# Performance work log

Hardware: AMD Instinct MI355X
Metric: run time of the kernel (lower is better)

The kernel has to match this reference:

```python
import jax, jax.numpy as jnp
import numpy as np

B, T, H, C = 131072, 40, 40, 4  # batch, seq_len (=input_size), hidden_size, classes


def setup_inputs() -> dict:
    key = jax.random.key(0)
    ks = jax.random.split(key, 7)
    s = 1.0 / np.sqrt(H)  # PyTorch LSTM/Linear init scale
    x = jax.random.normal(ks[0], (B, T), dtype=jnp.float32)
    W_ih = jax.random.uniform(ks[1], (4 * H, 1), jnp.float32, -s, s)
    W_hh = jax.random.uniform(ks[2], (4 * H, H), jnp.float32, -s, s)
    b_ih = jax.random.uniform(ks[3], (4 * H,), jnp.float32, -s, s)
    b_hh = jax.random.uniform(ks[4], (4 * H,), jnp.float32, -s, s)
    W_fc = jax.random.uniform(ks[5], (C, H), jnp.float32, -s, s)
    b_fc = jax.random.uniform(ks[6], (C,), jnp.float32, -s, s)
    return {"x": x, "W_ih": W_ih, "W_hh": W_hh, "b_ih": b_ih, "b_hh": b_hh,
            "W_fc": W_fc, "b_fc": b_fc}


def _lstm_last_hidden(x, W_ih, W_hh, b_ih, b_hh):
    # x: [B, T] -> per-step input is scalar feature. PyTorch gate order: i, f, g, o.
    b = b_ih + b_hh  # [4H]
    w_in = W_ih[:, 0]  # [4H] since input_size == 1
    h0 = jnp.zeros((x.shape[0], H), dtype=x.dtype)
    c0 = jnp.zeros((x.shape[0], H), dtype=x.dtype)

    def step(carry, x_t):
        h, c = carry
        # gates: [B, 4H]
        g = x_t[:, None] * w_in[None, :] + h @ W_hh.T + b
        i, f, gg, o = jnp.split(g, 4, axis=1)
        i = jax.nn.sigmoid(i)
        f = jax.nn.sigmoid(f)
        gg = jnp.tanh(gg)
        o = jax.nn.sigmoid(o)
        c_new = f * c + i * gg
        h_new = o * jnp.tanh(c_new)
        return (h_new, c_new), None

    (h_T, _), _ = jax.lax.scan(step, (h0, c0), x.T)  # scan over time (T steps)
    return h_T  # [B, H]


def reference(x, W_ih, W_hh, b_ih, b_hh, W_fc, b_fc):
    # Dropout(0.2) is identity in eval mode.
    h_T = _lstm_last_hidden(x, W_ih, W_hh, b_ih, b_hh)
    logits = h_T @ W_fc.T + b_fc  # [B, C]
    return logits, jnp.argmax(logits, axis=1)
```

## Files before the change

kernel.cpp:

```cpp
#include <hip/hip_runtime.h>


#define B_    131072
#define T_    40
#define H_    40
#define C_    4
#define BLK   256
#define WPB   4
#define SPW   16
#define SPB   64
#define LROW  68
#define NT    12
#define LOG2E 1.44269504088896340736f

typedef __fp16   fp16x2 __attribute__((ext_vector_type(2)));
typedef _Float16 half2v __attribute__((ext_vector_type(2)));
typedef _Float16 half4v __attribute__((ext_vector_type(4)));
typedef _Float16 half8v __attribute__((ext_vector_type(8)));
typedef float    f32x2  __attribute__((ext_vector_type(2)));
typedef float    f32x4  __attribute__((ext_vector_type(4)));

__device__ __forceinline__ float fexp2f(float v){ return __builtin_amdgcn_exp2f(v); }
__device__ __forceinline__ float frcpf (float v){ return __builtin_amdgcn_rcpf(v); }

__device__ __forceinline__ f32x2 fexp2v(f32x2 v){ return (f32x2){fexp2f(v[0]), fexp2f(v[1])}; }
__device__ __forceinline__ f32x2 frcpv (f32x2 v){ return (f32x2){frcpf(v[0]),  frcpf(v[1])};  }

__device__ __forceinline__ half2v pkrtz(float a, float b) {
    fp16x2 r = __builtin_amdgcn_cvt_pkrtz(a, b);
    return __builtin_bit_cast(half2v, r);
}

__device__ __forceinline__ float himask(float v) {
    return __builtin_bit_cast(float, __builtin_bit_cast(unsigned int, v) & 0xFFFFE000u);
}

__global__ __launch_bounds__(BLK, 2)
void lstm_mfma_kernel(const float* __restrict__ x,
                      const float* __restrict__ W_ih,
                      const float* __restrict__ W_hh,
                      const float* __restrict__ b_ih,
                      const float* __restrict__ b_hh,
                      const float* __restrict__ W_fc,
                      const float* __restrict__ b_fc,
                      float* __restrict__ out)
{
    __shared__ float lds[WPB * SPW * LROW];

    const int tid  = threadIdx.x;
    const int wv   = __builtin_amdgcn_readfirstlane(tid >> 6);
    const int lane = tid & 63;
    const int col  = lane & 15;
    const int quad = lane >> 4;
    const int sbase = blockIdx.x * SPB + wv * SPW;

    float* hbase = lds + wv * (SPW * LROW);

#pragma unroll
    for (int i = 0; i < (SPW * LROW) / 64; ++i)
        hbase[i * 64 + lane] = 0.0f;
    if (quad == 0) hbase[col * LROW + 41] = 1.0f;

    half8v Bh32[NT], Bl32[NT];
    half4v Bh16[NT], Bl16[NT];
#pragma unroll
    for (int tau = 0; tau < NT; ++tau) {
        const int   tt    = tau / 3;
        const int   ubase = (tau % 3) * 16;
        const float scale = (tt == 2) ? (2.0f * LOG2E) : (-LOG2E);
        const int   u     = ubase + col;
        const bool  valid = (u < H_);
        const int   r     = tt * H_ + (valid ? u : (H_ - 1));

        {
            float4 w0 = *reinterpret_cast<const float4*>(W_hh + r * H_ + 8 * quad);
            float4 w1 = *reinterpret_cast<const float4*>(W_hh + r * H_ + 8 * quad + 4);
            float wa[8] = {w0.x, w0.y, w0.z, w0.w, w1.x, w1.y, w1.z, w1.w};
            half8v bh, bl;
#pragma unroll
            for (int j = 0; j < 8; ++j) {
                float w = valid ? (wa[j] * scale) : 0.0f;
                _Float16 hi = (_Float16)w;
                bh[j] = hi;
                bl[j] = (_Float16)(w - (float)hi);
            }
            Bh32[tau] = bh; Bl32[tau] = bl;
        }
        {
            float4 wv4;
            if (quad == 0)      wv4 = *reinterpret_cast<const float4*>(W_hh + r * H_ + 32);
            else if (quad == 1) wv4 = *reinterpret_cast<const float4*>(W_hh + r * H_ + 36);
            else if (quad == 2) wv4 = make_float4(W_ih[r], b_ih[r] + b_hh[r], 0.0f, 0.0f);
            else                wv4 = make_float4(0.0f, 0.0f, 0.0f, 0.0f);
            float wa[4] = {wv4.x, wv4.y, wv4.z, wv4.w};
            half4v bh, bl;
#pragma unroll
            for (int j = 0; j < 4; ++j) {
                float w = valid ? (wa[j] * scale) : 0.0f;
                _Float16 hi = (_Float16)w;
                bh[j] = hi;
                bl[j] = (_Float16)(w - (float)hi);
            }
            Bh16[tau] = bh; Bl16[tau] = bl;
        }
    }

    f32x2 cst2[3][2];
#pragma unroll
    for (int jt = 0; jt < 3; ++jt) {
        cst2[jt][0] = (f32x2){0.f, 0.f};
        cst2[jt][1] = (f32x2){0.f, 0.f};
    }

    const f32x4 zc = (f32x4){0.f, 0.f, 0.f, 0.f};

    const float* myrow = hbase + col * LROW;
    const float* a32p  = myrow + 8 * quad;
    const float* a16p  = myrow + 32 + 4 * quad;
    float* xslot  = hbase + col * LROW + 40;
    float* wbase  = hbase + 4 * quad * LROW + col;
    float* wbase2 = wbase + ((col >= 8) ? 8 : 0);

    const float* xrow = x + (long)(sbase + col) * T_;
    float xv = xrow[0];

#pragma unroll 1
    for (int t = 0; t < T_; ++t) {
        if (quad == 0) *xslot = xv;
        const int tn = (t + 1 < T_) ? (t + 1) : (T_ - 1);
        const float xnext = xrow[tn];

        half8v ah32, al32; half4v ah16, al16;
        {
            f32x4 hv0 = *reinterpret_cast<const f32x4*>(a32p);
            f32x4 hv1 = *reinterpret_cast<const f32x4*>(a32p + 4);
            f32x4 hv2 = *reinterpret_cast<const f32x4*>(a16p);

            f32x4 hi0, hi1, hi2;
#pragma unroll
            for (int j = 0; j < 4; ++j) {
                hi0[j] = himask(hv0[j]);
                hi1[j] = himask(hv1[j]);
                hi2[j] = himask(hv2[j]);
            }
            f32x4 lo0 = hv0 - hi0;
            f32x4 lo1 = hv1 - hi1;
            f32x4 lo2 = hv2 - hi2;

            half2v h00 = pkrtz(hi0[0], hi0[1]);
            half2v h01 = pkrtz(hi0[2], hi0[3]);
            half2v h10 = pkrtz(hi1[0], hi1[1]);
            half2v h11 = pkrtz(hi1[2], hi1[3]);
            half2v l00 = pkrtz(lo0[0], lo0[1]);
            half2v l01 = pkrtz(lo0[2], lo0[3]);
            half2v l10 = pkrtz(lo1[0], lo1[1]);
            half2v l11 = pkrtz(lo1[2], lo1[3]);
            half2v h20 = pkrtz(hi2[0], hi2[1]);
            half2v h21 = pkrtz(hi2[2], hi2[3]);
            half2v l20 = pkrtz(lo2[0], lo2[1]);
            half2v l21 = pkrtz(lo2[2], lo2[3]);

            half4v a0 = __builtin_shufflevector(h00, h01, 0, 1, 2, 3);
            half4v a1 = __builtin_shufflevector(h10, h11, 0, 1, 2, 3);
            ah32 = __builtin_shufflevector(a0, a1, 0, 1, 2, 3, 4, 5, 6, 7);
            half4v b0 = __builtin_shufflevector(l00, l01, 0, 1, 2, 3);
            half4v b1 = __builtin_shufflevector(l10, l11, 0, 1, 2, 3);
            al32 = __builtin_shufflevector(b0, b1, 0, 1, 2, 3, 4, 5, 6, 7);
            ah16 = __builtin_shufflevector(h20, h21, 0, 1, 2, 3);
            al16 = __builtin_shufflevector(l20, l21, 0, 1, 2, 3);
        }

#pragma unroll
        for (int jt = 0; jt < 3; ++jt) {
#define DOT48(tau, dst)                                                          \
            {                                                                    \
                f32x4 a = __builtin_amdgcn_mfma_f32_16x16x32_f16(ah32, Bh32[tau], zc, 0, 0, 0); \
                a = __builtin_amdgcn_mfma_f32_16x16x32_f16(al32, Bh32[tau], a, 0, 0, 0); \
                a = __builtin_amdgcn_mfma_f32_16x16x32_f16(ah32, Bl32[tau], a, 0, 0, 0); \
                a = __builtin_amdgcn_mfma_f32_16x16x16f16(ah16, Bh16[tau], a, 0, 0, 0); \
                a = __builtin_amdgcn_mfma_f32_16x16x16f16(al16, Bh16[tau], a, 0, 0, 0); \
                a = __builtin_amdgcn_mfma_f32_16x16x16f16(ah16, Bl16[tau], a, 0, 0, 0); \
                dst = a;                                                         \
            }
            f32x4 ai, af, ag, ao;
            DOT48(jt, ai)
            DOT48(3 + jt, af)
            DOT48(6 + jt, ag)
            DOT48(9 + jt, ao)
#undef DOT48

#pragma unroll
            for (int p = 0; p < 2; ++p) {
                const f32x2 yi = (f32x2){ai[2*p], ai[2*p+1]};
                const f32x2 yf = (f32x2){af[2*p], af[2*p+1]};
                const f32x2 yg = (f32x2){ag[2*p], ag[2*p+1]};
                const f32x2 yo = (f32x2){ao[2*p], ao[2*p+1]};
                const f32x2 ei = fexp2v(yi);
                const f32x2 ef = fexp2v(yf);
                const f32x2 Eg = fexp2v(yg);
                const f32x2 eo = fexp2v(yo);
                const f32x2 one = (f32x2){1.0f, 1.0f};
                const f32x2 u_ = one + ei;
                const f32x2 v_ = one + Eg;
                const f32x2 w_ = one + ef;
                const f32x2 p_ = u_ * v_;
                const f32x2 q_ = (Eg - one) * w_;
                const f32x2 num = cst2[jt][p] * p_ + q_;
                const f32x2 cn  = num * frcpv(p_ * w_);
                cst2[jt][p] = cn;
                const f32x2 Ec = fexp2v(cn * (f32x2){2.0f*LOG2E, 2.0f*LOG2E});
                const f32x2 hn = (Ec - one) * frcpv((one + eo) * (one + Ec));
                if (jt < 2) {
                    wbase [(2*p)   * LROW + jt * 16] = hn[0];
                    wbase [(2*p+1) * LROW + jt * 16] = hn[1];
                } else {
                    wbase2[(2*p)   * LROW + 32]      = hn[0];
                    wbase2[(2*p+1) * LROW + 32]      = hn[1];
                }
            }
        }

        xv = xnext;
    }

    {
        float acc = b_fc[quad];
#pragma unroll
        for (int jj = 0; jj < 10; ++jj) {
            f32x4 hv = *reinterpret_cast<const f32x4*>(myrow + 4 * jj);
            float4 wv4 = *reinterpret_cast<const float4*>(W_fc + quad * H_ + 4 * jj);
            acc = fmaf(hv[0], wv4.x, acc);
            acc = fmaf(hv[1], wv4.y, acc);
            acc = fmaf(hv[2], wv4.z, acc);
            acc = fmaf(hv[3], wv4.w, acc);
        }
        out[(long)(sbase + col) * C_ + quad] = acc;
        hbase[col * LROW + 56 + quad] = acc;
    }
    if (quad == 0) {
        f32x4 lg = *reinterpret_cast<const f32x4*>(hbase + col * LROW + 56);
        int am = 0;
        float best = lg[0];
        if (lg[1] > best) { best = lg[1]; am = 1; }
        if (lg[2] > best) { best = lg[2]; am = 2; }
        if (lg[3] > best) { best = lg[3]; am = 3; }
        out[(long)B_ * C_ + sbase + col] = (float)am;
    }
}

extern "C" void kernel_launch(void* const* d_in, const int* in_sizes, int n_in,
                              void* d_out, int out_size, void* d_ws, size_t ws_size,
                              hipStream_t stream) {
    const float* x    = (const float*)d_in[0];
    const float* W_ih = (const float*)d_in[1];
    const float* W_hh = (const float*)d_in[2];
    const float* b_ih = (const float*)d_in[3];
    const float* b_hh = (const float*)d_in[4];
    const float* W_fc = (const float*)d_in[5];
    const float* b_fc = (const float*)d_in[6];
    float* out = (float*)d_out;

    dim3 block(BLK);
    dim3 grid(B_ / SPB);
    hipLaunchKernelGGL(lstm_mfma_kernel, grid, block, 0, stream,
                       x, W_ih, W_hh, b_ih, b_hh, W_fc, b_fc, out);
}
```

Measured before the change: 411.0 us.

## Process four independent 16-sample tiles per wave to interleave MFMA chains

Each wave now handles four independent 16-sample chunks at once, and loops twice over groups of them. The MFMA and activation work of the separate chains can interleave, hiding the dependency latency of each step's MFMA chain. The recurrent weight fragments are reused across more samples per load. The costs are higher register and LDS pressure, occupancy dropping to one block per SIMD budget, and fewer blocks in the grid.

New measurement: 456.4 us. +11.0%, slower.

```diff
diff --git a/kernel.cpp b/kernel.cpp
--- a/kernel.cpp
+++ b/kernel.cpp
@@ -7,9 +7,12 @@
 #define C_    4
 #define BLK   256
 #define WPB   4
-#define SPW   16
-#define SPB   64
-#define LROW  68
+#define NCH   4
+#define NGRP  2
+#define SPW   (NCH * 16)
+#define SPB   (WPB * SPW * NGRP)
+#define LROW  60
+#define TILEF (16 * LROW)
 #define NT    12
 #define LOG2E 1.44269504088896340736f
 
@@ -35,7 +38,85 @@
     return __builtin_bit_cast(float, __builtin_bit_cast(unsigned int, v) & 0xFFFFE000u);
 }
 
-__global__ __launch_bounds__(BLK, 2)
+__device__ __forceinline__ void prep_frags(const float* p32, const float* p16,
+                                           half8v& ah32, half8v& al32,
+                                           half4v& ah16, half4v& al16)
+{
+    f32x4 hv0 = *reinterpret_cast<const f32x4*>(p32);
+    f32x4 hv1 = *reinterpret_cast<const f32x4*>(p32 + 4);
+    f32x4 hv2 = *reinterpret_cast<const f32x4*>(p16);
+
+    f32x4 hi0, hi1, hi2;
+#pragma unroll
+    for (int j = 0; j < 4; ++j) {
+        hi0[j] = himask(hv0[j]);
+        hi1[j] = himask(hv1[j]);
+        hi2[j] = himask(hv2[j]);
+    }
+    f32x4 lo0 = hv0 - hi0;
+    f32x4 lo1 = hv1 - hi1;
+    f32x4 lo2 = hv2 - hi2;
+
+    half2v h00 = pkrtz(hi0[0], hi0[1]);
+    half2v h01 = pkrtz(hi0[2], hi0[3]);
+    half2v h10 = pkrtz(hi1[0], hi1[1]);
+    half2v h11 = pkrtz(hi1[2], hi1[3]);
+    half2v l00 = pkrtz(lo0[0], lo0[1]);
+    half2v l01 = pkrtz(lo0[2], lo0[3]);
+    half2v l10 = pkrtz(lo1[0], lo1[1]);
+    half2v l11 = pkrtz(lo1[2], lo1[3]);
+    half2v h20 = pkrtz(hi2[0], hi2[1]);
+    half2v h21 = pkrtz(hi2[2], hi2[3]);
+    half2v l20 = pkrtz(lo2[0], lo2[1]);
+    half2v l21 = pkrtz(lo2[2], lo2[3]);
+
+    half4v a0 = __builtin_shufflevector(h00, h01, 0, 1, 2, 3);
+    half4v a1 = __builtin_shufflevector(h10, h11, 0, 1, 2, 3);
+    ah32 = __builtin_shufflevector(a0, a1, 0, 1, 2, 3, 4, 5, 6, 7);
+    half4v b0 = __builtin_shufflevector(l00, l01, 0, 1, 2, 3);
+    half4v b1 = __builtin_shufflevector(l10, l11, 0, 1, 2, 3);
+    al32 = __builtin_shufflevector(b0, b1, 0, 1, 2, 3, 4, 5, 6, 7);
+    ah16 = __builtin_shufflevector(h20, h21, 0, 1, 2, 3);
+    al16 = __builtin_shufflevector(l20, l21, 0, 1, 2, 3);
+}
+
+__device__ __forceinline__ void gates_act(const f32x4& ai, const f32x4& af,
+                                          const f32x4& ag, const f32x4& ao,
+                                          f32x2 (&cst)[2],
+                                          float* wb, float* wb2, const int jt)
+{
+#pragma unroll
+    for (int p = 0; p < 2; ++p) {
+        const f32x2 yi = (f32x2){ai[2*p], ai[2*p+1]};
+        const f32x2 yf = (f32x2){af[2*p], af[2*p+1]};
+        const f32x2 yg = (f32x2){ag[2*p], ag[2*p+1]};
+        const f32x2 yo = (f32x2){ao[2*p], ao[2*p+1]};
+        const f32x2 ei = fexp2v(yi);
+        const f32x2 ef = fexp2v(yf);
+        const f32x2 Eg = fexp2v(yg);
+        const f32x2 eo = fexp2v(yo);
+        const f32x2 one = (f32x2){1.0f, 1.0f};
+        const f32x2 u_ = one + ei;
+        const f32x2 v_ = one + Eg;
+        const f32x2 w_ = one + ef;
+        const f32x2 p_ = u_ * v_;
+        const f32x2 q_ = (Eg - one) * w_;
+        const f32x2 num = cst[p] * p_ + q_;
+        const f32x2 cn  = num * frcpv(p_ * w_);
+        cst[p] = cn;
+        const f32x2 Ec = fexp2v(cn * (f32x2){2.0f*LOG2E, 2.0f*LOG2E});
+        const f32x2 hn = (Ec - one) * frcpv((one + eo) * (one + Ec));
+        if (jt < 2) {
+            wb [(2*p)   * LROW + jt * 16] = hn[0];
+            wb [(2*p+1) * LROW + jt * 16] = hn[1];
+        } else {
+            wb2[(2*p)   * LROW + 32]      = hn[0];
+            wb2[(2*p+1) * LROW + 32]      = hn[1];
+        }
+    }
+}
+
+__global__ __launch_bounds__(BLK, 1)
 void lstm_mfma_kernel(const float* __restrict__ x,
                       const float* __restrict__ W_ih,
                       const float* __restrict__ W_hh,
@@ -45,21 +126,15 @@
                       const float* __restrict__ b_fc,
                       float* __restrict__ out)
 {
-    __shared__ float lds[WPB * SPW * LROW];
+    __shared__ __align__(16) float lds[WPB * NCH * TILEF];
 
     const int tid  = threadIdx.x;
     const int wv   = __builtin_amdgcn_readfirstlane(tid >> 6);
     const int lane = tid & 63;
     const int col  = lane & 15;
     const int quad = lane >> 4;
-    const int sbase = blockIdx.x * SPB + wv * SPW;
-
-    float* hbase = lds + wv * (SPW * LROW);
-
-#pragma unroll
-    for (int i = 0; i < (SPW * LROW) / 64; ++i)
-        hbase[i * 64 + lane] = 0.0f;
-    if (quad == 0) hbase[col * LROW + 41] = 1.0f;
+
+    float* hbase = lds + wv * (NCH * TILEF);
 
     half8v Bh32[NT], Bl32[NT];
     half4v Bh16[NT], Bl16[NT];
@@ -105,146 +180,108 @@
         }
     }
 
-    f32x2 cst2[3][2];
-#pragma unroll
-    for (int jt = 0; jt < 3; ++jt) {
-        cst2[jt][0] = (f32x2){0.f, 0.f};
-        cst2[jt][1] = (f32x2){0.f, 0.f};
-    }
-
     const f32x4 zc = (f32x4){0.f, 0.f, 0.f, 0.f};
 
-    const float* myrow = hbase + col * LROW;
-    const float* a32p  = myrow + 8 * quad;
-    const float* a16p  = myrow + 32 + 4 * quad;
-    float* xslot  = hbase + col * LROW + 40;
-    float* wbase  = hbase + 4 * quad * LROW + col;
-    float* wbase2 = wbase + ((col >= 8) ? 8 : 0);
-
-    const float* xrow = x + (long)(sbase + col) * T_;
-    float xv = xrow[0];
+    const float* pA   = hbase + col * LROW + 8 * quad;
+    const float* pA16 = hbase + col * LROW + 32 + 4 * quad;
+    float* pX   = hbase + quad * TILEF + col * LROW + 40;
+    float* pW   = hbase + 4 * quad * LROW + col;
+    float* pW2  = pW + ((col >= 8) ? 8 : 0);
+    float* pRow = hbase + col * LROW;
+
+    const long wavebase = (long)blockIdx.x * SPB + (long)wv * (SPW * NGRP);
 
 #pragma unroll 1
-    for (int t = 0; t < T_; ++t) {
-        if (quad == 0) *xslot = xv;
-        const int tn = (t + 1 < T_) ? (t + 1) : (T_ - 1);
-        const float xnext = xrow[tn];
-
-        half8v ah32, al32; half4v ah16, al16;
+    for (int g = 0; g < NGRP; ++g) {
+        const long gbase = wavebase + (long)g * SPW;
+
         {
-            f32x4 hv0 = *reinterpret_cast<const f32x4*>(a32p);
-            f32x4 hv1 = *reinterpret_cast<const f32x4*>(a32p + 4);
-            f32x4 hv2 = *reinterpret_cast<const f32x4*>(a16p);
-
-            f32x4 hi0, hi1, hi2;
-#pragma unroll
-            for (int j = 0; j < 4; ++j) {
-                hi0[j] = himask(hv0[j]);
-                hi1[j] = himask(hv1[j]);
-                hi2[j] = himask(hv2[j]);
-            }
-            f32x4 lo0 = hv0 - hi0;
-            f32x4 lo1 = hv1 - hi1;
-            f32x4 lo2 = hv2 - hi2;
-
-            half2v h00 = pkrtz(hi0[0], hi0[1]);
-            half2v h01 = pkrtz(hi0[2], hi0[3]);
-            half2v h10 = pkrtz(hi1[0], hi1[1]);
-            half2v h11 = pkrtz(hi1[2], hi1[3]);
-            half2v l00 = pkrtz(lo0[0], lo0[1]);
-            half2v l01 = pkrtz(lo0[2], lo0[3]);
-            half2v l10 = pkrtz(lo1[0], lo1[1]);
-            half2v l11 = pkrtz(lo1[2], lo1[3]);
-            half2v h20 = pkrtz(hi2[0], hi2[1]);
-            half2v h21 = pkrtz(hi2[2], hi2[3]);
-            half2v l20 = pkrtz(lo2[0], lo2[1]);
-            half2v l21 = pkrtz(lo2[2], lo2[3]);
-
-            half4v a0 = __builtin_shufflevector(h00, h01, 0, 1, 2, 3);
-            half4v a1 = __builtin_shufflevector(h10, h11, 0, 1, 2, 3);
-            ah32 = __builtin_shufflevector(a0, a1, 0, 1, 2, 3, 4, 5, 6, 7);
-            half4v b0 = __builtin_shufflevector(l00, l01, 0, 1, 2, 3);
-            half4v b1 = __builtin_shufflevector(l10, l11, 0, 1, 2, 3);
-            al32 = __builtin_shufflevector(b0, b1, 0, 1, 2, 3, 4, 5, 6, 7);
-            ah16 = __builtin_shufflevector(h20, h21, 0, 1, 2, 3);
-            al16 = __builtin_shufflevector(l20, l21, 0, 1, 2, 3);
-        }
-
-#pragma unroll
-        for (int jt = 0; jt < 3; ++jt) {
+            f32x4* zp = reinterpret_cast<f32x4*>(hbase);
+#pragma unroll
+            for (int i = 0; i < (NCH * TILEF) / 4 / 64; ++i)
+                zp[i * 64 + lane] = zc;
+            hbase[quad * TILEF + col * LROW + 41] = 1.0f;
+        }
+
+        f32x2 cst2[NCH][3][2];
+#pragma unroll
+        for (int c = 0; c < NCH; ++c)
+#pragma unroll
+            for (int jt = 0; jt < 3; ++jt) {
+                cst2[c][jt][0] = (f32x2){0.f, 0.f};
+                cst2[c][jt][1] = (f32x2){0.f, 0.f};
+            }
+
+        const float* xs = x + (long)(gbase + quad * 16 + col) * T_;
+        float xv = xs[0];
+
+#pragma unroll 1
+        for (int t = 0; t < T_; ++t) {
+            *pX = xv;
+            const int tn = (t + 1 < T_) ? (t + 1) : (T_ - 1);
+            const float xnext = xs[tn];
+
+            half8v ah32[NCH], al32[NCH]; half4v ah16[NCH], al16[NCH];
+#pragma unroll
+            for (int c = 0; c < NCH; ++c)
+                prep_frags(pA + c * TILEF, pA16 + c * TILEF,
+                           ah32[c], al32[c], ah16[c], al16[c]);
+
+#pragma unroll
+            for (int jt = 0; jt < 3; ++jt) {
+#pragma unroll
+                for (int c = 0; c < NCH; ++c) {
 #define DOT48(tau, dst)                                                          \
-            {                                                                    \
-                f32x4 a = __builtin_amdgcn_mfma_f32_16x16x32_f16(ah32, Bh32[tau], zc, 0, 0, 0); \
-                a = __builtin_amdgcn_mfma_f32_16x16x32_f16(al32, Bh32[tau], a, 0, 0, 0); \
-                a = __builtin_amdgcn_mfma_f32_16x16x32_f16(ah32, Bl32[tau], a, 0, 0, 0); \
-                a = __builtin_amdgcn_mfma_f32_16x16x16f16(ah16, Bh16[tau], a, 0, 0, 0); \
-                a = __builtin_amdgcn_mfma_f32_16x16x16f16(al16, Bh16[tau], a, 0, 0, 0); \
-                a = __builtin_amdgcn_mfma_f32_16x16x16f16(ah16, Bl16[tau], a, 0, 0, 0); \
-                dst = a;                                                         \
-            }
-            f32x4 ai, af, ag, ao;
-            DOT48(jt, ai)
-            DOT48(3 + jt, af)
-            DOT48(6 + jt, ag)
-            DOT48(9 + jt, ao)
+                    {                                                            \
+                        f32x4 a_ = __builtin_amdgcn_mfma_f32_16x16x32_f16(ah32[c], Bh32[tau], zc, 0, 0, 0); \
+                        a_ = __builtin_amdgcn_mfma_f32_16x16x32_f16(al32[c], Bh32[tau], a_, 0, 0, 0); \
+                        a_ = __builtin_amdgcn_mfma_f32_16x16x32_f16(ah32[c], Bl32[tau], a_, 0, 0, 0); \
+                        a_ = __builtin_amdgcn_mfma_f32_16x16x16f16(ah16[c], Bh16[tau], a_, 0, 0, 0); \
+                        a_ = __builtin_amdgcn_mfma_f32_16x16x16f16(al16[c], Bh16[tau], a_, 0, 0, 0); \
+                        a_ = __builtin_amdgcn_mfma_f32_16x16x16f16(ah16[c], Bl16[tau], a_, 0, 0, 0); \
+                        dst = a_;                                                \
+                    }
+                    f32x4 ai, af, ag, ao;
+                    DOT48(jt,     ai)
+                    DOT48(3 + jt, af)
+                    DOT48(6 + jt, ag)
+                    DOT48(9 + jt, ao)
 #undef DOT48
-
-#pragma unroll
-            for (int p = 0; p < 2; ++p) {
-                const f32x2 yi = (f32x2){ai[2*p], ai[2*p+1]};
-                const f32x2 yf = (f32x2){af[2*p], af[2*p+1]};
-                const f32x2 yg = (f32x2){ag[2*p], ag[2*p+1]};
-                const f32x2 yo = (f32x2){ao[2*p], ao[2*p+1]};
-                const f32x2 ei = fexp2v(yi);
-                const f32x2 ef = fexp2v(yf);
-                const f32x2 Eg = fexp2v(yg);
-                const f32x2 eo = fexp2v(yo);
-                const f32x2 one = (f32x2){1.0f, 1.0f};
-                const f32x2 u_ = one + ei;
-                const f32x2 v_ = one + Eg;
-                const f32x2 w_ = one + ef;
-                const f32x2 p_ = u_ * v_;
-                const f32x2 q_ = (Eg - one) * w_;
-                const f32x2 num = cst2[jt][p] * p_ + q_;
-                const f32x2 cn  = num * frcpv(p_ * w_);
-                cst2[jt][p] = cn;
-                const f32x2 Ec = fexp2v(cn * (f32x2){2.0f*LOG2E, 2.0f*LOG2E});
-                const f32x2 hn = (Ec - one) * frcpv((one + eo) * (one + Ec));
-                if (jt < 2) {
-                    wbase [(2*p)   * LROW + jt * 16] = hn[0];
-                    wbase [(2*p+1) * LROW + jt * 16] = hn[1];
-                } else {
-                    wbase2[(2*p)   * LROW + 32]      = hn[0];
-                    wbase2[(2*p+1) * LROW + 32]      = hn[1];
+                    gates_act(ai, af, ag, ao, cst2[c][jt],
+                              pW + c * TILEF, pW2 + c * TILEF, jt);
                 }
             }
-        }
-
-        xv = xnext;
-    }
-
-    {
-        float acc = b_fc[quad];
-#pragma unroll
-        for (int jj = 0; jj < 10; ++jj) {
-            f32x4 hv = *reinterpret_cast<const f32x4*>(myrow + 4 * jj);
-            float4 wv4 = *reinterpret_cast<const float4*>(W_fc + quad * H_ + 4 * jj);
-            acc = fmaf(hv[0], wv4.x, acc);
-            acc = fmaf(hv[1], wv4.y, acc);
-            acc = fmaf(hv[2], wv4.z, acc);
-            acc = fmaf(hv[3], wv4.w, acc);
-        }
-        out[(long)(sbase + col) * C_ + quad] = acc;
-        hbase[col * LROW + 56 + quad] = acc;
-    }
-    if (quad == 0) {
-        f32x4 lg = *reinterpret_cast<const f32x4*>(hbase + col * LROW + 56);
-        int am = 0;
-        float best = lg[0];
-        if (lg[1] > best) { best = lg[1]; am = 1; }
-        if (lg[2] > best) { best = lg[2]; am = 2; }
-        if (lg[3] > best) { best = lg[3]; am = 3; }
-        out[(long)B_ * C_ + sbase + col] = (float)am;
+
+            xv = xnext;
+        }
+
+#pragma unroll
+        for (int c = 0; c < NCH; ++c) {
+            float acc = b_fc[quad];
+#pragma unroll
+            for (int jj = 0; jj < 10; ++jj) {
+                f32x4 hv = *reinterpret_cast<const f32x4*>(pRow + c * TILEF + 4 * jj);
+                float4 wv4 = *reinterpret_cast<const float4*>(W_fc + quad * H_ + 4 * jj);
+                acc = fmaf(hv[0], wv4.x, acc);
+                acc = fmaf(hv[1], wv4.y, acc);
+                acc = fmaf(hv[2], wv4.z, acc);
+                acc = fmaf(hv[3], wv4.w, acc);
+            }
+            out[(long)(gbase + c * 16 + col) * C_ + quad] = acc;
+            pRow[c * TILEF + 56 + quad] = acc;
+        }
+        if (quad == 0) {
+#pragma unroll
+            for (int c = 0; c < NCH; ++c) {
+                f32x4 lg = *reinterpret_cast<const f32x4*>(pRow + c * TILEF + 56);
+                int am = 0;
+                float best = lg[0];
+                if (lg[1] > best) { best = lg[1]; am = 1; }
+                if (lg[2] > best) { best = lg[2]; am = 2; }
+                if (lg[3] > best) { best = lg[3]; am = 3; }
+                out[(long)B_ * C_ + gbase + c * 16 + col] = (float)am;
+            }
+        }
     }
 }
 
```

## Pack tail hidden units into two gate tiles and reload h early

Applied to the files above, without the earlier changes.

The last 8 hidden units (32..39) are now packed so that one 16-column MFMA tile carries the i and f gates and another carries g and o, with lane-xor-8 shuffles exchanging the partner values. This cuts the weight tiles from 12 to 10, which removes two 6-MFMA groups per timestep that previously ran on padded zero columns. The next step's h loads are also moved up to right after the LDS writes they depend on, and the x slot store is moved, so the loads can overlap with the remaining math. The cost is cross-lane shuffles and more subtle ordering. Reading LDS without barriers relies on the per-wave layout, and the earlier loads must stay ordered after the matching writes.

Result: faster. 381.1 us (-7.3%).

```diff
diff --git a/kernel.cpp b/kernel.cpp
--- a/kernel.cpp
+++ b/kernel.cpp
@@ -10,7 +10,7 @@
 #define SPW   16
 #define SPB   64
 #define LROW  68
-#define NT    12
+#define NT    10
 #define LOG2E 1.44269504088896340736f
 
 typedef __fp16   fp16x2 __attribute__((ext_vector_type(2)));
@@ -26,6 +26,10 @@
 __device__ __forceinline__ f32x2 fexp2v(f32x2 v){ return (f32x2){fexp2f(v[0]), fexp2f(v[1])}; }
 __device__ __forceinline__ f32x2 frcpv (f32x2 v){ return (f32x2){frcpf(v[0]),  frcpf(v[1])};  }
 
+__device__ __forceinline__ f32x2 shflx8(f32x2 v){
+    return (f32x2){ __shfl_xor(v[0], 8, 64), __shfl_xor(v[1], 8, 64) };
+}
+
 __device__ __forceinline__ half2v pkrtz(float a, float b) {
     fp16x2 r = __builtin_amdgcn_cvt_pkrtz(a, b);
     return __builtin_bit_cast(half2v, r);
@@ -33,6 +37,37 @@
 
 __device__ __forceinline__ float himask(float v) {
     return __builtin_bit_cast(float, __builtin_bit_cast(unsigned int, v) & 0xFFFFE000u);
+}
+
+__device__ __forceinline__ void gates_act(const f32x4& ai, const f32x4& af,
+                                          const f32x4& ag, const f32x4& ao,
+                                          f32x2 (&cst)[2],
+                                          float* wb, const int jt)
+{
+#pragma unroll
+    for (int p = 0; p < 2; ++p) {
+        const f32x2 yi = (f32x2){ai[2*p], ai[2*p+1]};
+        const f32x2 yf = (f32x2){af[2*p], af[2*p+1]};
+        const f32x2 yg = (f32x2){ag[2*p], ag[2*p+1]};
+        const f32x2 yo = (f32x2){ao[2*p], ao[2*p+1]};
+        const f32x2 ei = fexp2v(yi);
+        const f32x2 ef = fexp2v(yf);
+        const f32x2 Eg = fexp2v(yg);
+        const f32x2 eo = fexp2v(yo);
+        const f32x2 one = (f32x2){1.0f, 1.0f};
+        const f32x2 u_ = one + ei;
+        const f32x2 v_ = one + Eg;
+        const f32x2 w_ = one + ef;
+        const f32x2 p_ = u_ * v_;
+        const f32x2 q_ = (Eg - one) * w_;
+        const f32x2 num = cst[p] * p_ + q_;
+        const f32x2 cn  = num * frcpv(p_ * w_);
+        cst[p] = cn;
+        const f32x2 Ec = fexp2v(cn * (f32x2){2.0f*LOG2E, 2.0f*LOG2E});
+        const f32x2 hn = (Ec - one) * frcpv((one + eo) * (one + Ec));
+        wb[(2*p)   * LROW + jt * 16] = hn[0];
+        wb[(2*p+1) * LROW + jt * 16] = hn[1];
+    }
 }
 
 __global__ __launch_bounds__(BLK, 2)
@@ -65,12 +100,20 @@
     half4v Bh16[NT], Bl16[NT];
 #pragma unroll
     for (int tau = 0; tau < NT; ++tau) {
-        const int   tt    = tau / 3;
-        const int   ubase = (tau % 3) * 16;
-        const float scale = (tt == 2) ? (2.0f * LOG2E) : (-LOG2E);
-        const int   u     = ubase + col;
-        const bool  valid = (u < H_);
-        const int   r     = tt * H_ + (valid ? u : (H_ - 1));
+        int   r;
+        float scale;
+        if (tau < 8) {
+            const int tt = tau >> 1;
+            const int jt = tau & 1;
+            r     = tt * H_ + jt * 16 + col;
+            scale = (tt == 2) ? (2.0f * LOG2E) : (-LOG2E);
+        } else if (tau == 8) {
+            r     = (col < 8) ? (32 + col) : (H_ + 32 + (col - 8));
+            scale = -LOG2E;
+        } else {
+            r     = (col < 8) ? (2 * H_ + 32 + col) : (3 * H_ + 32 + (col - 8));
+            scale = (col < 8) ? (2.0f * LOG2E) : (-LOG2E);
+        }
 
         {
             float4 w0 = *reinterpret_cast<const float4*>(W_hh + r * H_ + 8 * quad);
@@ -79,7 +122,7 @@
             half8v bh, bl;
 #pragma unroll
             for (int j = 0; j < 8; ++j) {
-                float w = valid ? (wa[j] * scale) : 0.0f;
+                float w = wa[j] * scale;
                 _Float16 hi = (_Float16)w;
                 bh[j] = hi;
                 bl[j] = (_Float16)(w - (float)hi);
@@ -96,7 +139,7 @@
             half4v bh, bl;
 #pragma unroll
             for (int j = 0; j < 4; ++j) {
-                float w = valid ? (wa[j] * scale) : 0.0f;
+                float w = wa[j] * scale;
                 _Float16 hi = (_Float16)w;
                 bh[j] = hi;
                 bl[j] = (_Float16)(w - (float)hi);
@@ -119,23 +162,23 @@
     const float* a16p  = myrow + 32 + 4 * quad;
     float* xslot  = hbase + col * LROW + 40;
     float* wbase  = hbase + 4 * quad * LROW + col;
-    float* wbase2 = wbase + ((col >= 8) ? 8 : 0);
+    float* wbase2 = wbase + ((col >= 8) ? 8 : 0) + 32;
 
     const float* xrow = x + (long)(sbase + col) * T_;
     float xv = xrow[0];
+    if (quad == 0) *xslot = xv;
+
+    f32x4 hv0 = *reinterpret_cast<const f32x4*>(a32p);
+    f32x4 hv1 = *reinterpret_cast<const f32x4*>(a32p + 4);
+    f32x4 hv2 = *reinterpret_cast<const f32x4*>(a16p);
 
 #pragma unroll 1
     for (int t = 0; t < T_; ++t) {
-        if (quad == 0) *xslot = xv;
         const int tn = (t + 1 < T_) ? (t + 1) : (T_ - 1);
         const float xnext = xrow[tn];
 
         half8v ah32, al32; half4v ah16, al16;
         {
-            f32x4 hv0 = *reinterpret_cast<const f32x4*>(a32p);
-            f32x4 hv1 = *reinterpret_cast<const f32x4*>(a32p + 4);
-            f32x4 hv2 = *reinterpret_cast<const f32x4*>(a16p);
-
             f32x4 hi0, hi1, hi2;
 #pragma unroll
             for (int j = 0; j < 4; ++j) {
@@ -170,57 +213,60 @@
             al16 = __builtin_shufflevector(l20, l21, 0, 1, 2, 3);
         }
 
-#pragma unroll
-        for (int jt = 0; jt < 3; ++jt) {
 #define DOT48(tau, dst)                                                          \
-            {                                                                    \
-                f32x4 a = __builtin_amdgcn_mfma_f32_16x16x32_f16(ah32, Bh32[tau], zc, 0, 0, 0); \
-                a = __builtin_amdgcn_mfma_f32_16x16x32_f16(al32, Bh32[tau], a, 0, 0, 0); \
-                a = __builtin_amdgcn_mfma_f32_16x16x32_f16(ah32, Bl32[tau], a, 0, 0, 0); \
-                a = __builtin_amdgcn_mfma_f32_16x16x16f16(ah16, Bh16[tau], a, 0, 0, 0); \
-                a = __builtin_amdgcn_mfma_f32_16x16x16f16(al16, Bh16[tau], a, 0, 0, 0); \
-                a = __builtin_amdgcn_mfma_f32_16x16x16f16(ah16, Bl16[tau], a, 0, 0, 0); \
-                dst = a;                                                         \
+        {                                                                        \
+            f32x4 a_ = __builtin_amdgcn_mfma_f32_16x16x32_f16(ah32, Bh32[tau], zc, 0, 0, 0); \
+            a_ = __builtin_amdgcn_mfma_f32_16x16x32_f16(al32, Bh32[tau], a_, 0, 0, 0); \
+            a_ = __builtin_amdgcn_mfma_f32_16x16x32_f16(ah32, Bl32[tau], a_, 0, 0, 0); \
+            a_ = __builtin_amdgcn_mfma_f32_16x16x16f16(ah16, Bh16[tau], a_, 0, 0, 0); \
+            a_ = __builtin_amdgcn_mfma_f32_16x16x16f16(al16, Bh16[tau], a_, 0, 0, 0); \
+            a_ = __builtin_amdgcn_mfma_f32_16x16x16f16(ah16, Bl16[tau], a_, 0, 0, 0); \
+            dst = a_;                                                            \
+        }
+
+#pragma unroll
+        for (int jt = 0; jt < 2; ++jt) {
+            f32x4 ai, af, ag, ao;
+            DOT48(0 + jt, ai)
+            DOT48(2 + jt, af)
+            DOT48(4 + jt, ag)
+            DOT48(6 + jt, ao)
+            gates_act(ai, af, ag, ao, cst2[jt], wbase, jt);
+        }
+
+        hv0 = *reinterpret_cast<const f32x4*>(a32p);
+        hv1 = *reinterpret_cast<const f32x4*>(a32p + 4);
+
+        {
+            f32x4 aif, ago;
+            DOT48(8, aif)
+            DOT48(9, ago)
+#pragma unroll
+            for (int p = 0; p < 2; ++p) {
+                const f32x2 y1 = (f32x2){aif[2*p], aif[2*p+1]};
+                const f32x2 y2 = (f32x2){ago[2*p], ago[2*p+1]};
+                const f32x2 e1 = fexp2v(y1);
+                const f32x2 e2 = fexp2v(y2);
+                const f32x2 one = (f32x2){1.0f, 1.0f};
+                const f32x2 s1 = one + e1;
+                const f32x2 s2 = one + e2;
+                const f32x2 w_ = shflx8(s1);
+                const f32x2 oe = shflx8(s2);
+                const f32x2 p_ = s1 * s2;
+                const f32x2 q_ = (e2 - one) * w_;
+                const f32x2 num = cst2[2][p] * p_ + q_;
+                const f32x2 cn  = num * frcpv(p_ * w_);
+                cst2[2][p] = cn;
+                const f32x2 Ec = fexp2v(cn * (f32x2){2.0f*LOG2E, 2.0f*LOG2E});
+                const f32x2 hn = (Ec - one) * frcpv(oe * (one + Ec));
+                wbase2[(2*p)   * LROW] = hn[0];
+                wbase2[(2*p+1) * LROW] = hn[1];
             }
-            f32x4 ai, af, ag, ao;
-            DOT48(jt, ai)
-            DOT48(3 + jt, af)
-            DOT48(6 + jt, ag)
-            DOT48(9 + jt, ao)
+        }
+
+        if (quad == 0) *xslot = xnext;
+        hv2 = *reinterpret_cast<const f32x4*>(a16p);
 #undef DOT48
-
-#pragma unroll
-            for (int p = 0; p < 2; ++p) {
-                const f32x2 yi = (f32x2){ai[2*p], ai[2*p+1]};
-                const f32x2 yf = (f32x2){af[2*p], af[2*p+1]};
-                const f32x2 yg = (f32x2){ag[2*p], ag[2*p+1]};
-                const f32x2 yo = (f32x2){ao[2*p], ao[2*p+1]};
-                const f32x2 ei = fexp2v(yi);
-                const f32x2 ef = fexp2v(yf);
-                const f32x2 Eg = fexp2v(yg);
-                const f32x2 eo = fexp2v(yo);
-                const f32x2 one = (f32x2){1.0f, 1.0f};
-                const f32x2 u_ = one + ei;
-                const f32x2 v_ = one + Eg;
-                const f32x2 w_ = one + ef;
-                const f32x2 p_ = u_ * v_;
-                const f32x2 q_ = (Eg - one) * w_;
-                const f32x2 num = cst2[jt][p] * p_ + q_;
-                const f32x2 cn  = num * frcpv(p_ * w_);
-                cst2[jt][p] = cn;
-                const f32x2 Ec = fexp2v(cn * (f32x2){2.0f*LOG2E, 2.0f*LOG2E});
-                const f32x2 hn = (Ec - one) * frcpv((one + eo) * (one + Ec));
-                if (jt < 2) {
-                    wbase [(2*p)   * LROW + jt * 16] = hn[0];
-                    wbase [(2*p+1) * LROW + jt * 16] = hn[1];
-                } else {
-                    wbase2[(2*p)   * LROW + 32]      = hn[0];
-                    wbase2[(2*p+1) * LROW + 32]      = hn[1];
-                }
-            }
-        }
-
-        xv = xnext;
     }
 
     {
```
